# Performance work log

Measured on AMD Instinct MI355X. Metric: run time of the kernel, lower is better.

The kernel has to match this reference:

```python
import jax, jax.numpy as jnp
import numpy as np

N = 1_500_000  # nodes (250k tracklets x 6 hits)
E = 12_000_000  # edges


def setup_inputs() -> dict:
    key = jax.random.key(0)
    ks = jax.random.split(key, 26)
    w = lambda k, shape: (jax.random.normal(k, shape, jnp.float32) * 0.1)
    inp = {
        "x": jax.random.normal(ks[0], (N, 1), jnp.float32),
        "edge_index": jax.random.randint(ks[1], (2, E), 0, N),
        "edge_attr": jax.random.normal(ks[2], (E, 2), jnp.float32),
        # conv1: in=1, prop=9, edge=2, out=9
        "Wx1": w(ks[3], (9, 1)), "bx1": w(ks[4], (9,)),
        "We1": w(ks[5], (9, 2)), "be1": w(ks[6], (9,)),
        "Wo1": w(ks[7], (9, 9)), "bo1": w(ks[8], (9,)),
        # conv2: in=9, prop=9, edge=2, out=9
        "Wx2": w(ks[9], (9, 9)), "bx2": w(ks[10], (9,)),
        "We2": w(ks[11], (9, 2)), "be2": w(ks[12], (9,)),
        "Wo2": w(ks[13], (9, 9)), "bo2": w(ks[14], (9,)),
        # conv3: in=9, prop=9, edge=2, out=4
        "Wx3": w(ks[15], (9, 9)), "bx3": w(ks[16], (9,)),
        "We3": w(ks[17], (9, 2)), "be3": w(ks[18], (9,)),
        "Wo3": w(ks[19], (4, 9)), "bo3": w(ks[20], (4,)),
        # head MLP
        "W1": w(ks[21], (8, 24)), "b1": w(ks[22], (8,)),
        "W2": w(ks[23], (4, 8)), "b2": w(ks[24], (4,)),
    }
    return inp


def _conv(x, src, dst, edge_attr, Wx, bx, We, be, Wo, bo):
    # trackletGNN: lin_x -> gather x_j -> * lin_edge(edge_attr) -> scatter-add -> lin_out
    h = x @ Wx.T + bx                      # [N, P]
    msg = h[src] * (edge_attr @ We.T + be)  # [E, P] gather + edge linear + multiply
    agg = jax.ops.segment_sum(msg, dst, num_segments=x.shape[0])  # [N, P]
    return agg @ Wo.T + bo


def reference(x, edge_index, edge_attr,
              Wx1, bx1, We1, be1, Wo1, bo1,
              Wx2, bx2, We2, be2, Wo2, bo2,
              Wx3, bx3, We3, be3, Wo3, bo3,
              W1, b1, W2, b2):
    src, dst = edge_index[0], edge_index[1]
    h = jax.nn.relu(_conv(x, src, dst, edge_attr, Wx1, bx1, We1, be1, Wo1, bo1))
    h = jax.nn.relu(_conv(h, src, dst, edge_attr, Wx2, bx2, We2, be2, Wo2, bo2))
    h = jax.nn.relu(_conv(h, src, dst, edge_attr, Wx3, bx3, We3, be3, Wo3, bo3))
    h = h.reshape(-1, 24)                   # 6 nodes x 4 feats per tracklet
    h = jax.nn.relu(h @ W1.T + b1)
    h = h @ W2.T + b2
    return jax.nn.log_softmax(h, axis=1)
```

## Files before the change

kernel.cpp:

```cpp
#include <hip/hip_runtime.h>
#include <hip/hip_bf16.h>


#define NNODES 1500000
#define NEDGES 12000000
#define NTRACK 250000
#define NBUCK  1465
#define PCHUNK 4096
#define PBLK   2930
#define HCHUNK 32768
#define HBLK   367
#define SRCMASK 0x1FFFFFu
#define FXSCALE 16777216.f
#define FXINV   (1.f / 16777216.f)

typedef unsigned int   u32;
typedef unsigned short u16;

static __device__ __forceinline__ float b2f(u32 v) {
    union { float f; u32 u; } x; x.u = v << 16; return x.f;
}
static __device__ __forceinline__ u16 f2b(float f) {
    __hip_bfloat16 h = __float2bfloat16(f);
    return *reinterpret_cast<u16*>(&h);
}
static __device__ __forceinline__ float ldw(const void* p, int i, int isf32) {
    return isf32 ? ((const float*)p)[i] : b2f((u32)((const u16*)p)[i]);
}
static __device__ __forceinline__ int fx(float f) {
    return (int)rintf(f * FXSCALE);
}


__global__ void k_detect(const u16* a, const u16* b, const u16* c,
                         const u16* d, const u16* e, const u16* f,
                         int* flag) {
    if (blockIdx.x == 0 && threadIdx.x == 0) {
        int isf32 = 0;
        const u16* ps[6] = {a, b, c, d, e, f};
        const int  ns[6] = {9, 9, 9, 9, 9, 8};
        for (int k = 0; k < 6; k++)
            for (int i = 0; i < ns[k]; i++) {
                float v = b2f((u32)ps[k][i]);
                if (!(fabsf(v) < 1.0e3f)) isf32 = 1;
            }
        *flag = isf32;
    }
}


__global__ __launch_bounds__(256) void k_xcast(const void* __restrict__ x,
                                               u16* __restrict__ xb,
                                               const int* __restrict__ flag) {
    int isf32 = *flag;
    int n = blockIdx.x * 256 + threadIdx.x;
    if (n < NNODES)
        xb[n] = isf32 ? f2b(((const float*)x)[n]) : ((const u16*)x)[n];
}


__global__ __launch_bounds__(512) void k_bhist(const int* __restrict__ dst,
                                               int* __restrict__ gh) {
    __shared__ u32 h[NBUCK];
    int t = threadIdx.x;
    for (int b = t; b < NBUCK; b += 512) h[b] = 0;
    __syncthreads();
    int c0 = blockIdx.x * HCHUNK;
#pragma unroll 4
    for (int i = 0; i < HCHUNK / 512; i++) {
        int e = c0 + i * 512 + t;
        if (e < NEDGES) atomicAdd(&h[((u32)dst[e]) >> 10], 1u);
    }
    __syncthreads();
    for (int b = t; b < NBUCK; b += 512) {
        u32 c = h[b];
        if (c) atomicAdd((u32*)&gh[b], c);
    }
}

__global__ __launch_bounds__(256) void k_bscan(const int* __restrict__ gh,
                                               int* __restrict__ bstart,
                                               int* __restrict__ gcur) {
    __shared__ u32 sd[256];
    __shared__ u32 carry;
    int t = threadIdx.x;
    if (t == 0) carry = 0;
    __syncthreads();
    for (int c0 = 0; c0 < NBUCK; c0 += 256) {
        int b = c0 + t;
        u32 v = (b < NBUCK) ? (u32)gh[b] : 0;
        sd[t] = v; __syncthreads();
        for (int o = 1; o < 256; o <<= 1) {
            u32 a = (t >= o) ? sd[t - o] : 0;
            __syncthreads();
            sd[t] += a;
            __syncthreads();
        }
        u32 excl = carry + sd[t] - v;
        if (b < NBUCK) { bstart[b] = (int)excl; gcur[b] = (int)excl; }
        __syncthreads();
        if (t == 255) carry += sd[255];
        __syncthreads();
    }
    if (t == 0) bstart[NBUCK] = NEDGES;
}


__global__ __launch_bounds__(512) void k_part(const int* __restrict__ src,
                                              const int* __restrict__ dst,
                                              const void* __restrict__ attr,
                                              int* __restrict__ gcur,
                                              uint2* __restrict__ perm,
                                              const int* __restrict__ flag) {
    __shared__ int   cur[NBUCK];
    __shared__ int   gbA[NBUCK];
    __shared__ uint2 rec[PCHUNK];
    __shared__ u32   gad[PCHUNK];
    __shared__ u32   sd[512];
    __shared__ u32   carryS;
    int isf32 = *flag;
    int t = threadIdx.x;
    int c0 = blockIdx.x * PCHUNK;
    int chunkN = NEDGES - c0; if (chunkN > PCHUNK) chunkN = PCHUNK;

    for (int b = t; b < NBUCK; b += 512) cur[b] = 0;
    if (t == 0) carryS = 0;
    __syncthreads();

    int ds_[8], sr_[8];
#pragma unroll
    for (int k = 0; k < 8; k++) {
        int e = c0 + k * 512 + t;
        if (e < NEDGES) {
            ds_[k] = dst[e];
            sr_[k] = src[e];
            atomicAdd((u32*)&cur[((u32)ds_[k]) >> 10], 1u);
        } else { ds_[k] = -1; sr_[k] = 0; }
    }
    __syncthreads();

    for (int b0 = 0; b0 < NBUCK; b0 += 512) {
        int b = b0 + t;
        u32 v = (b < NBUCK) ? (u32)cur[b] : 0;
        sd[t] = v; __syncthreads();
        for (int o = 1; o < 512; o <<= 1) {
            u32 a = (t >= o) ? sd[t - o] : 0;
            __syncthreads();
            sd[t] += a;
            __syncthreads();
        }
        u32 excl = carryS + sd[t] - v;
        if (b < NBUCK) {
            cur[b] = (int)excl;
            if (v) gbA[b] = atomicAdd(&gcur[b], (int)v) - (int)excl;
        }
        __syncthreads();
        if (t == 511) carryS += sd[511];
        __syncthreads();
    }

#pragma unroll
    for (int k = 0; k < 8; k++) {
        int e = c0 + k * 512 + t;
        if (e < NEDGES) {
            u32 d  = (u32)ds_[k];
            u32 fb = d >> 10;
            u32 ap;
            if (isf32) {
                float2 a = ((const float2*)attr)[e];
                ap = (u32)f2b(a.x) | ((u32)f2b(a.y) << 16);
            } else {
                ap = ((const u32*)attr)[e];
            }
            int slot = atomicAdd(&cur[fb], 1);
            uint2 r; r.x = ((u32)sr_[k]) | ((d & 1023u) << 21); r.y = ap;
            rec[slot] = r;
            gad[slot] = (u32)(gbA[fb] + slot);
        }
    }
    __syncthreads();

#pragma unroll
    for (int j = 0; j < 8; j++) {
        int s = j * 512 + t;
        if (s < chunkN) perm[gad[s]] = rec[s];
    }
}


__global__ __launch_bounds__(256) void k_eagg1(
        const int* __restrict__ bstart, const uint2* __restrict__ perm,
        const u16* __restrict__ xb,
        const void* Wx, const void* bx, const void* We, const void* be,
        const void* Wo, const void* bo, const void* Wxn, const void* bxn,
        uint4* __restrict__ hA, u16* __restrict__ hB,
        const int* __restrict__ flag) {
    __shared__ int acc[1024 * 9];
    __shared__ float sWx[9], sbx[9], sWe[18], sbe[9], sWo[81], sbo[9], sWxn[81], sbxn[9];
    int isf32 = *flag;
    int t = threadIdx.x;
    if (t < 9)  sWx[t]  = ldw(Wx,  t, isf32);
    if (t < 9)  sbx[t]  = ldw(bx,  t, isf32);
    if (t < 18) sWe[t]  = ldw(We,  t, isf32);
    if (t < 9)  sbe[t]  = ldw(be,  t, isf32);
    if (t < 81) sWo[t]  = ldw(Wo,  t, isf32);
    if (t < 9)  sbo[t]  = ldw(bo,  t, isf32);
    if (t < 81) sWxn[t] = ldw(Wxn, t, isf32);
    if (t < 9)  sbxn[t] = ldw(bxn, t, isf32);
    for (int i = t; i < 1024 * 9; i += 256) acc[i] = 0;
    __syncthreads();

    int b = blockIdx.x;
    int r0 = bstart[b], r1 = bstart[b + 1];
    for (int i = r0 + t; i < r1; i += 256) {
        uint2 rec = perm[i];
        int   l   = (int)((rec.x >> 21) & 1023u);
        float xs  = b2f((u32)xb[rec.x & SRCMASK]);
        float a0  = b2f(rec.y & 0xffffu);
        float a1  = b2f(rec.y >> 16);
        int* ap = &acc[l * 9];
#pragma unroll
        for (int j = 0; j < 9; j++) {
            float e  = fmaf(a0, sWe[2 * j], fmaf(a1, sWe[2 * j + 1], sbe[j]));
            float hh = fmaf(xs, sWx[j], sbx[j]);
            atomicAdd(&ap[j], fx(hh * e));
        }
    }
    __syncthreads();

    for (int l = t; l < 1024; l += 256) {
        int n = b * 1024 + l;
        if (n >= NNODES) break;
        float av[9];
#pragma unroll
        for (int j = 0; j < 9; j++) av[j] = (float)acc[l * 9 + j] * FXINV;
        float o[9];
#pragma unroll
        for (int k = 0; k < 9; k++) {
            float v = sbo[k];
#pragma unroll
            for (int j = 0; j < 9; j++) v = fmaf(av[j], sWo[k * 9 + j], v);
            o[k] = fmaxf(v, 0.f);
        }
        u16 hv[9];
#pragma unroll
        for (int j = 0; j < 9; j++) {
            float v = sbxn[j];
#pragma unroll
            for (int k = 0; k < 9; k++) v = fmaf(o[k], sWxn[j * 9 + k], v);
            hv[j] = f2b(v);
        }
        uint4 q;
        q.x = (u32)hv[0] | ((u32)hv[1] << 16);
        q.y = (u32)hv[2] | ((u32)hv[3] << 16);
        q.z = (u32)hv[4] | ((u32)hv[5] << 16);
        q.w = (u32)hv[6] | ((u32)hv[7] << 16);
        hA[n] = q;
        hB[n] = hv[8];
    }
}


template <int OUTF, bool FUSE_NEXT>
__global__ __launch_bounds__(256) void k_eagg(
        const int* __restrict__ bstart, const uint2* __restrict__ perm,
        const uint4* __restrict__ hA, const u16* __restrict__ hB,
        const void* We, const void* be, const void* Wo, const void* bo,
        const void* Wxn, const void* bxn,
        uint4* __restrict__ oA, u16* __restrict__ oB,
        const int* __restrict__ flag) {
    __shared__ int acc[1024 * 9];
    __shared__ float sWe[18], sbe[9], sWo[OUTF * 9], sbo[OUTF], sWxn[81], sbxn[9];
    int isf32 = *flag;
    int t = threadIdx.x;
    if (t < 18)       sWe[t] = ldw(We, t, isf32);
    if (t < 9)        sbe[t] = ldw(be, t, isf32);
    if (t < OUTF * 9) sWo[t] = ldw(Wo, t, isf32);
    if (t < OUTF)     sbo[t] = ldw(bo, t, isf32);
    if constexpr (FUSE_NEXT) {
        if (t < 81) sWxn[t] = ldw(Wxn, t, isf32);
        if (t < 9)  sbxn[t] = ldw(bxn, t, isf32);
    }
    for (int i = t; i < 1024 * 9; i += 256) acc[i] = 0;
    __syncthreads();

    int b = blockIdx.x;
    int r0 = bstart[b], r1 = bstart[b + 1];
    for (int i = r0 + t; i < r1; i += 256) {
        uint2 rec = perm[i];
        int   s   = (int)(rec.x & SRCMASK);
        int   l   = (int)((rec.x >> 21) & 1023u);
        float a0  = b2f(rec.y & 0xffffu);
        float a1  = b2f(rec.y >> 16);
        uint4 qa  = hA[s];
        u32   qb  = (u32)hB[s];
        float h[9];
        h[0] = b2f(qa.x & 0xffffu); h[1] = b2f(qa.x >> 16);
        h[2] = b2f(qa.y & 0xffffu); h[3] = b2f(qa.y >> 16);
        h[4] = b2f(qa.z & 0xffffu); h[5] = b2f(qa.z >> 16);
        h[6] = b2f(qa.w & 0xffffu); h[7] = b2f(qa.w >> 16);
        h[8] = b2f(qb);
        int* ap = &acc[l * 9];
#pragma unroll
        for (int j = 0; j < 9; j++) {
            float e = fmaf(a0, sWe[2 * j], fmaf(a1, sWe[2 * j + 1], sbe[j]));
            atomicAdd(&ap[j], fx(h[j] * e));
        }
    }
    __syncthreads();

    for (int l = t; l < 1024; l += 256) {
        int n = b * 1024 + l;
        if (n >= NNODES) break;
        float av[9];
#pragma unroll
        for (int j = 0; j < 9; j++) av[j] = (float)acc[l * 9 + j] * FXINV;
        float o[OUTF];
#pragma unroll
        for (int k = 0; k < OUTF; k++) {
            float v = sbo[k];
#pragma unroll
            for (int j = 0; j < 9; j++) v = fmaf(av[j], sWo[k * 9 + j], v);
            o[k] = fmaxf(v, 0.f);
        }
        if constexpr (FUSE_NEXT) {
            u16 hv[9];
#pragma unroll
            for (int j = 0; j < 9; j++) {
                float v = sbxn[j];
#pragma unroll
                for (int k = 0; k < OUTF; k++) v = fmaf(o[k], sWxn[j * 9 + k], v);
                hv[j] = f2b(v);
            }
            uint4 q;
            q.x = (u32)hv[0] | ((u32)hv[1] << 16);
            q.y = (u32)hv[2] | ((u32)hv[3] << 16);
            q.z = (u32)hv[4] | ((u32)hv[5] << 16);
            q.w = (u32)hv[6] | ((u32)hv[7] << 16);
            oA[n] = q;
            oB[n] = hv[8];
        } else {
            uint2 q;
            q.x = (u32)f2b(o[0]) | ((u32)f2b(o[1]) << 16);
            q.y = (u32)f2b(o[2]) | ((u32)f2b(o[3]) << 16);
            ((uint2*)oA)[n] = q;
        }
    }
}


__global__ __launch_bounds__(256) void k_head(
        const u16* __restrict__ f,
        const void* W1, const void* b1, const void* W2, const void* b2,
        void* __restrict__ out, const int* __restrict__ flag) {
    __shared__ float sW1[192], sb1[8], sW2[32], sb2[4];
    int isf32 = *flag;
    int t = threadIdx.x;
    if (t < 192) sW1[t] = ldw(W1, t, isf32);
    if (t < 8)   sb1[t] = ldw(b1, t, isf32);
    if (t < 32)  sW2[t] = ldw(W2, t, isf32);
    if (t < 4)   sb2[t] = ldw(b2, t, isf32);
    __syncthreads();

    int tr = blockIdx.x * 256 + t;
    if (tr >= NTRACK) return;

    const uint4* fp = (const uint4*)(f + (size_t)tr * 24);
    uint4 A = fp[0], B = fp[1], C = fp[2];
    u32 w[12] = {A.x, A.y, A.z, A.w, B.x, B.y, B.z, B.w, C.x, C.y, C.z, C.w};
    float in[24];
#pragma unroll
    for (int i = 0; i < 12; i++) {
        in[2 * i]     = b2f(w[i] & 0xffffu);
        in[2 * i + 1] = b2f(w[i] >> 16);
    }

    float z1[8];
#pragma unroll
    for (int o = 0; o < 8; o++) {
        float v = sb1[o];
#pragma unroll
        for (int i = 0; i < 24; i++) v = fmaf(in[i], sW1[o * 24 + i], v);
        z1[o] = fmaxf(v, 0.f);
    }
    float z2[4];
#pragma unroll
    for (int c = 0; c < 4; c++) {
        float v = sb2[c];
#pragma unroll
        for (int o = 0; o < 8; o++) v = fmaf(z1[o], sW2[c * 8 + o], v);
        z2[c] = v;
    }
    float m = fmaxf(fmaxf(z2[0], z2[1]), fmaxf(z2[2], z2[3]));
    float s = 0.f;
#pragma unroll
    for (int c = 0; c < 4; c++) s += expf(z2[c] - m);
    float l = logf(s) + m;

    if (isf32) {
        float4 q; q.x = z2[0] - l; q.y = z2[1] - l; q.z = z2[2] - l; q.w = z2[3] - l;
        ((float4*)((float*)out + (size_t)tr * 4))[0] = q;
    } else {
        uint2 q;
        q.x = (u32)f2b(z2[0] - l) | ((u32)f2b(z2[1] - l) << 16);
        q.y = (u32)f2b(z2[2] - l) | ((u32)f2b(z2[3] - l) << 16);
        ((uint2*)((u16*)out + (size_t)tr * 4))[0] = q;
    }
}


extern "C" void kernel_launch(void* const* d_in, const int* in_sizes, int n_in,
                              void* d_out, int out_size, void* d_ws, size_t ws_size,
                              hipStream_t stream) {
    const void* X    = d_in[0];
    const int* eidx  = (const int*)d_in[1];
    const void* eattr= d_in[2];
    const void *WX1 = d_in[3],  *BX1 = d_in[4];
    const void *WE1 = d_in[5],  *BE1 = d_in[6];
    const void *WO1 = d_in[7],  *BO1 = d_in[8];
    const void *WX2 = d_in[9],  *BX2 = d_in[10];
    const void *WE2 = d_in[11], *BE2 = d_in[12];
    const void *WO2 = d_in[13], *BO2 = d_in[14];
    const void *WX3 = d_in[15], *BX3 = d_in[16];
    const void *WE3 = d_in[17], *BE3 = d_in[18];
    const void *WO3 = d_in[19], *BO3 = d_in[20];
    const void *W1  = d_in[21], *B1  = d_in[22];
    const void *W2  = d_in[23], *B2  = d_in[24];

    const int* src = eidx;
    const int* dst = eidx + NEDGES;

    char* w = (char*)d_ws;
    size_t off = 0;
    auto take = [&](size_t bytes) -> void* {
        void* p = w + off;
        off += (bytes + 255) & ~(size_t)255;
        return p;
    };
    int*   flag   = (int*)take(256);
    int*   gh     = (int*)take((size_t)NBUCK * 4);
    int*   bstart = (int*)take((size_t)(NBUCK + 1) * 4);
    int*   gcur   = (int*)take((size_t)NBUCK * 4);
    u16*   xb     = (u16*)take((size_t)NNODES * 2);
    uint2* perm   = (uint2*)take((size_t)NEDGES * 8);
    uint4* hA2    = (uint4*)take((size_t)NNODES * 16);
    u16*   hB2    = (u16*)take((size_t)NNODES * 2);
    uint4* hA3    = (uint4*)take((size_t)NNODES * 16);
    u16*   hB3    = (u16*)take((size_t)NNODES * 2);
    u16*   f      = (u16*)hA2;
    (void)ws_size; (void)n_in; (void)in_sizes; (void)out_size;

    const int NB = (NNODES + 255) / 256;
    const int TB = (NTRACK + 255) / 256;

    hipMemsetAsync(gh, 0, (size_t)NBUCK * 4, stream);

    k_detect <<<1,    64,  0, stream>>>((const u16*)BX1, (const u16*)BE1, (const u16*)BO1,
                                        (const u16*)BX2, (const u16*)BE2, (const u16*)B1, flag);
    k_xcast  <<<NB,   256, 0, stream>>>(X, xb, flag);
    k_bhist  <<<HBLK, 512, 0, stream>>>(dst, gh);
    k_bscan  <<<1,    256, 0, stream>>>(gh, bstart, gcur);
    k_part   <<<PBLK, 512, 0, stream>>>(src, dst, eattr, gcur, perm, flag);

    k_eagg1        <<<NBUCK, 256, 0, stream>>>(bstart, perm, xb,
                                               WX1, BX1, WE1, BE1, WO1, BO1, WX2, BX2,
                                               hA2, hB2, flag);
    k_eagg<9,true> <<<NBUCK, 256, 0, stream>>>(bstart, perm, hA2, hB2,
                                               WE2, BE2, WO2, BO2, WX3, BX3,
                                               hA3, hB3, flag);
    k_eagg<4,false><<<NBUCK, 256, 0, stream>>>(bstart, perm, hA3, hB3,
                                               WE3, BE3, WO3, BO3, WO3, BO3,
                                               (uint4*)f, (u16*)f, flag);
    k_head         <<<TB,    256, 0, stream>>>(f, W1, B1, W2, B2, d_out, flag);
}
```

Baseline: 1.124 ms.

## Halve bucket size, interleave node features, drop partition address buffer

Buckets shrink from 1024 to 512 destination nodes, so the per-block LDS accumulator halves and more blocks can be resident (launch bounds now request 8 blocks). Node features move from split 16-byte plus 2-byte arrays into one interleaved 32-byte record per node, so each gather touches a single contiguous region instead of two arrays. The partition kernel drops its shared global-address array and finds each slot's bucket by binary search over the scanned offsets. The edge-linear term is computed before the gather is consumed. This trades LDS and memory footprint for extra binary-search work and a larger intermediate feature buffer.

```diff
diff --git a/kernel.cpp b/kernel.cpp
--- a/kernel.cpp
+++ b/kernel.cpp
@@ -5,7 +5,10 @@
 #define NNODES 1500000
 #define NEDGES 12000000
 #define NTRACK 250000
-#define NBUCK  1465
+#define BSH    9
+#define BSZ    512
+#define BMASK  511u
+#define NBUCK  2930
 #define PCHUNK 4096
 #define PBLK   2930
 #define HCHUNK 32768
@@ -69,7 +72,7 @@
 #pragma unroll 4
     for (int i = 0; i < HCHUNK / 512; i++) {
         int e = c0 + i * 512 + t;
-        if (e < NEDGES) atomicAdd(&h[((u32)dst[e]) >> 10], 1u);
+        if (e < NEDGES) atomicAdd(&h[((u32)dst[e]) >> BSH], 1u);
     }
     __syncthreads();
     for (int b = t; b < NBUCK; b += 512) {
@@ -115,7 +118,6 @@
     __shared__ int   cur[NBUCK];
     __shared__ int   gbA[NBUCK];
     __shared__ uint2 rec[PCHUNK];
-    __shared__ u32   gad[PCHUNK];
     __shared__ u32   sd[512];
     __shared__ u32   carryS;
     int isf32 = *flag;
@@ -134,7 +136,7 @@
         if (e < NEDGES) {
             ds_[k] = dst[e];
             sr_[k] = src[e];
-            atomicAdd((u32*)&cur[((u32)ds_[k]) >> 10], 1u);
+            atomicAdd((u32*)&cur[((u32)ds_[k]) >> BSH], 1u);
         } else { ds_[k] = -1; sr_[k] = 0; }
     }
     __syncthreads();
@@ -164,7 +166,7 @@
         int e = c0 + k * 512 + t;
         if (e < NEDGES) {
             u32 d  = (u32)ds_[k];
-            u32 fb = d >> 10;
+            u32 fb = d >> BSH;
             u32 ap;
             if (isf32) {
                 float2 a = ((const float2*)attr)[e];
@@ -173,9 +175,8 @@
                 ap = ((const u32*)attr)[e];
             }
             int slot = atomicAdd(&cur[fb], 1);
-            uint2 r; r.x = ((u32)sr_[k]) | ((d & 1023u) << 21); r.y = ap;
+            uint2 r; r.x = ((u32)sr_[k]) | ((d & BMASK) << 21); r.y = ap;
             rec[slot] = r;
-            gad[slot] = (u32)(gbA[fb] + slot);
         }
     }
     __syncthreads();
@@ -183,19 +184,25 @@
 #pragma unroll
     for (int j = 0; j < 8; j++) {
         int s = j * 512 + t;
-        if (s < chunkN) perm[gad[s]] = rec[s];
-    }
-}
-
-
-__global__ __launch_bounds__(256) void k_eagg1(
+        if (s < chunkN) {
+            int lo = 0, hi = NBUCK - 1;
+            while (lo < hi) {
+                int mid = (lo + hi) >> 1;
+                if (cur[mid] > s) hi = mid; else lo = mid + 1;
+            }
+            perm[gbA[lo] + s] = rec[s];
+        }
+    }
+}
+
+
+__global__ __launch_bounds__(256, 8) void k_eagg1(
         const int* __restrict__ bstart, const uint2* __restrict__ perm,
         const u16* __restrict__ xb,
         const void* Wx, const void* bx, const void* We, const void* be,
         const void* Wo, const void* bo, const void* Wxn, const void* bxn,
-        uint4* __restrict__ hA, u16* __restrict__ hB,
-        const int* __restrict__ flag) {
-    __shared__ int acc[1024 * 9];
+        uint4* __restrict__ hO, const int* __restrict__ flag) {
+    __shared__ int acc[BSZ * 9];
     __shared__ float sWx[9], sbx[9], sWe[18], sbe[9], sWo[81], sbo[9], sWxn[81], sbxn[9];
     int isf32 = *flag;
     int t = threadIdx.x;
@@ -207,14 +214,14 @@
     if (t < 9)  sbo[t]  = ldw(bo,  t, isf32);
     if (t < 81) sWxn[t] = ldw(Wxn, t, isf32);
     if (t < 9)  sbxn[t] = ldw(bxn, t, isf32);
-    for (int i = t; i < 1024 * 9; i += 256) acc[i] = 0;
+    for (int i = t; i < BSZ * 9; i += 256) acc[i] = 0;
     __syncthreads();
 
     int b = blockIdx.x;
     int r0 = bstart[b], r1 = bstart[b + 1];
     for (int i = r0 + t; i < r1; i += 256) {
         uint2 rec = perm[i];
-        int   l   = (int)((rec.x >> 21) & 1023u);
+        int   l   = (int)((rec.x >> 21) & BMASK);
         float xs  = b2f((u32)xb[rec.x & SRCMASK]);
         float a0  = b2f(rec.y & 0xffffu);
         float a1  = b2f(rec.y >> 16);
@@ -228,8 +235,8 @@
     }
     __syncthreads();
 
-    for (int l = t; l < 1024; l += 256) {
-        int n = b * 1024 + l;
+    for (int l = t; l < BSZ; l += 256) {
+        int n = b * BSZ + l;
         if (n >= NNODES) break;
         float av[9];
 #pragma unroll
@@ -250,27 +257,28 @@
             for (int k = 0; k < 9; k++) v = fmaf(o[k], sWxn[j * 9 + k], v);
             hv[j] = f2b(v);
         }
-        uint4 q;
-        q.x = (u32)hv[0] | ((u32)hv[1] << 16);
-        q.y = (u32)hv[2] | ((u32)hv[3] << 16);
-        q.z = (u32)hv[4] | ((u32)hv[5] << 16);
-        q.w = (u32)hv[6] | ((u32)hv[7] << 16);
-        hA[n] = q;
-        hB[n] = hv[8];
+        uint4 q0, q1;
+        q0.x = (u32)hv[0] | ((u32)hv[1] << 16);
+        q0.y = (u32)hv[2] | ((u32)hv[3] << 16);
+        q0.z = (u32)hv[4] | ((u32)hv[5] << 16);
+        q0.w = (u32)hv[6] | ((u32)hv[7] << 16);
+        q1.x = (u32)hv[8]; q1.y = 0; q1.z = 0; q1.w = 0;
+        size_t p = (size_t)n << 1;
+        hO[p] = q0; hO[p + 1] = q1;
     }
 }
 
 
 template <int OUTF, bool FUSE_NEXT>
-__global__ __launch_bounds__(256) void k_eagg(
+__global__ __launch_bounds__(256, 8) void k_eagg(
         const int* __restrict__ bstart, const uint2* __restrict__ perm,
-        const uint4* __restrict__ hA, const u16* __restrict__ hB,
+        const uint4* __restrict__ hT,
         const void* We, const void* be, const void* Wo, const void* bo,
         const void* Wxn, const void* bxn,
-        uint4* __restrict__ oA, u16* __restrict__ oB,
-        const int* __restrict__ flag) {
-    __shared__ int acc[1024 * 9];
-    __shared__ float sWe[18], sbe[9], sWo[OUTF * 9], sbo[OUTF], sWxn[81], sbxn[9];
+        uint4* __restrict__ oT, const int* __restrict__ flag) {
+    __shared__ int acc[BSZ * 9];
+    __shared__ float sWe[18], sbe[9], sWo[OUTF * 9], sbo[OUTF];
+    __shared__ float sWxn[FUSE_NEXT ? 81 : 1], sbxn[FUSE_NEXT ? 9 : 1];
     int isf32 = *flag;
     int t = threadIdx.x;
     if (t < 18)       sWe[t] = ldw(We, t, isf32);
@@ -281,7 +289,7 @@
         if (t < 81) sWxn[t] = ldw(Wxn, t, isf32);
         if (t < 9)  sbxn[t] = ldw(bxn, t, isf32);
     }
-    for (int i = t; i < 1024 * 9; i += 256) acc[i] = 0;
+    for (int i = t; i < BSZ * 9; i += 256) acc[i] = 0;
     __syncthreads();
 
     int b = blockIdx.x;
@@ -289,28 +297,31 @@
     for (int i = r0 + t; i < r1; i += 256) {
         uint2 rec = perm[i];
         int   s   = (int)(rec.x & SRCMASK);
-        int   l   = (int)((rec.x >> 21) & 1023u);
+        const uint4* hp = hT + ((size_t)s << 1);
+        uint4 qa  = hp[0];
+        u32   qb  = hp[1].x;
+        int   l   = (int)((rec.x >> 21) & BMASK);
         float a0  = b2f(rec.y & 0xffffu);
         float a1  = b2f(rec.y >> 16);
-        uint4 qa  = hA[s];
-        u32   qb  = (u32)hB[s];
+        float ev[9];
+#pragma unroll
+        for (int j = 0; j < 9; j++)
+            ev[j] = fmaf(a0, sWe[2 * j], fmaf(a1, sWe[2 * j + 1], sbe[j]));
         float h[9];
         h[0] = b2f(qa.x & 0xffffu); h[1] = b2f(qa.x >> 16);
         h[2] = b2f(qa.y & 0xffffu); h[3] = b2f(qa.y >> 16);
         h[4] = b2f(qa.z & 0xffffu); h[5] = b2f(qa.z >> 16);
         h[6] = b2f(qa.w & 0xffffu); h[7] = b2f(qa.w >> 16);
-        h[8] = b2f(qb);
+        h[8] = b2f(qb & 0xffffu);
         int* ap = &acc[l * 9];
 #pragma unroll
-        for (int j = 0; j < 9; j++) {
-            float e = fmaf(a0, sWe[2 * j], fmaf(a1, sWe[2 * j + 1], sbe[j]));
-            atomicAdd(&ap[j], fx(h[j] * e));
-        }
-    }
-    __syncthreads();
-
-    for (int l = t; l < 1024; l += 256) {
-        int n = b * 1024 + l;
+        for (int j = 0; j < 9; j++)
+            atomicAdd(&ap[j], fx(h[j] * ev[j]));
+    }
+    __syncthreads();
+
+    for (int l = t; l < BSZ; l += 256) {
+        int n = b * BSZ + l;
         if (n >= NNODES) break;
         float av[9];
 #pragma unroll
@@ -332,18 +343,19 @@
                 for (int k = 0; k < OUTF; k++) v = fmaf(o[k], sWxn[j * 9 + k], v);
                 hv[j] = f2b(v);
             }
-            uint4 q;
-            q.x = (u32)hv[0] | ((u32)hv[1] << 16);
-            q.y = (u32)hv[2] | ((u32)hv[3] << 16);
-            q.z = (u32)hv[4] | ((u32)hv[5] << 16);
-            q.w = (u32)hv[6] | ((u32)hv[7] << 16);
-            oA[n] = q;
-            oB[n] = hv[8];
+            uint4 q0, q1;
+            q0.x = (u32)hv[0] | ((u32)hv[1] << 16);
+            q0.y = (u32)hv[2] | ((u32)hv[3] << 16);
+            q0.z = (u32)hv[4] | ((u32)hv[5] << 16);
+            q0.w = (u32)hv[6] | ((u32)hv[7] << 16);
+            q1.x = (u32)hv[8]; q1.y = 0; q1.z = 0; q1.w = 0;
+            size_t p = (size_t)n << 1;
+            oT[p] = q0; oT[p + 1] = q1;
         } else {
             uint2 q;
             q.x = (u32)f2b(o[0]) | ((u32)f2b(o[1]) << 16);
             q.y = (u32)f2b(o[2]) | ((u32)f2b(o[3]) << 16);
-            ((uint2*)oA)[n] = q;
+            ((uint2*)oT)[n] = q;
         }
     }
 }
@@ -443,11 +455,9 @@
     int*   gcur   = (int*)take((size_t)NBUCK * 4);
     u16*   xb     = (u16*)take((size_t)NNODES * 2);
     uint2* perm   = (uint2*)take((size_t)NEDGES * 8);
-    uint4* hA2    = (uint4*)take((size_t)NNODES * 16);
-    u16*   hB2    = (u16*)take((size_t)NNODES * 2);
-    uint4* hA3    = (uint4*)take((size_t)NNODES * 16);
-    u16*   hB3    = (u16*)take((size_t)NNODES * 2);
-    u16*   f      = (u16*)hA2;
+    uint4* h2     = (uint4*)take((size_t)NNODES * 32);
+    uint4* h3     = (uint4*)take((size_t)NNODES * 32);
+    u16*   f      = (u16*)h2;
     (void)ws_size; (void)n_in; (void)in_sizes; (void)out_size;
 
     const int NB = (NNODES + 255) / 256;
@@ -464,12 +474,12 @@
 
     k_eagg1        <<<NBUCK, 256, 0, stream>>>(bstart, perm, xb,
                                                WX1, BX1, WE1, BE1, WO1, BO1, WX2, BX2,
-                                               hA2, hB2, flag);
-    k_eagg<9,true> <<<NBUCK, 256, 0, stream>>>(bstart, perm, hA2, hB2,
+                                               h2, flag);
+    k_eagg<9,true> <<<NBUCK, 256, 0, stream>>>(bstart, perm, h2,
                                                WE2, BE2, WO2, BO2, WX3, BX3,
-                                               hA3, hB3, flag);
-    k_eagg<4,false><<<NBUCK, 256, 0, stream>>>(bstart, perm, hA3, hB3,
+                                               h3, flag);
+    k_eagg<4,false><<<NBUCK, 256, 0, stream>>>(bstart, perm, h3,
                                                WE3, BE3, WO3, BO3, WO3, BO3,
-                                               (uint4*)f, (u16*)f, flag);
+                                               (uint4*)f, flag);
     k_head         <<<TB,    256, 0, stream>>>(f, W1, B1, W2, B2, d_out, flag);
 }
```

Result: slower. 1.642 ms (+46.1%).

## Halve dst bucket size and sort each bucket's edges by source slice

Applied to the files above, without the earlier changes.

Shrinks destination buckets from 1024 to 512 nodes, which doubles the block count for the aggregation kernels and halves their shared accumulator. It adds a per-bucket counting-sort pass (k_srt) that reorders edges by source-index slice so the gathers of hA/hB in later layers have more locality. The partition kernel now finds each record's bucket by binary search over the shared prefix array instead of storing a per-slot global address, which frees shared memory. In exchange it adds an extra read and write pass over the 12M-edge permutation, and buckets longer than 5120 edges are silently left unsorted.

```diff
diff --git a/kernel.cpp b/kernel.cpp
--- a/kernel.cpp
+++ b/kernel.cpp
@@ -5,12 +5,17 @@
 #define NNODES 1500000
 #define NEDGES 12000000
 #define NTRACK 250000
-#define NBUCK  1465
+#define BSH    9
+#define BSZ    512
+#define BMASK  511u
+#define NBUCK  2930
 #define PCHUNK 4096
 #define PBLK   2930
 #define HCHUNK 32768
 #define HBLK   367
 #define SRCMASK 0x1FFFFFu
+#define NSLICE 48
+#define SRTR   20
 #define FXSCALE 16777216.f
 #define FXINV   (1.f / 16777216.f)
 
@@ -69,7 +74,7 @@
 #pragma unroll 4
     for (int i = 0; i < HCHUNK / 512; i++) {
         int e = c0 + i * 512 + t;
-        if (e < NEDGES) atomicAdd(&h[((u32)dst[e]) >> 10], 1u);
+        if (e < NEDGES) atomicAdd(&h[((u32)dst[e]) >> BSH], 1u);
     }
     __syncthreads();
     for (int b = t; b < NBUCK; b += 512) {
@@ -115,7 +120,6 @@
     __shared__ int   cur[NBUCK];
     __shared__ int   gbA[NBUCK];
     __shared__ uint2 rec[PCHUNK];
-    __shared__ u32   gad[PCHUNK];
     __shared__ u32   sd[512];
     __shared__ u32   carryS;
     int isf32 = *flag;
@@ -134,7 +138,7 @@
         if (e < NEDGES) {
             ds_[k] = dst[e];
             sr_[k] = src[e];
-            atomicAdd((u32*)&cur[((u32)ds_[k]) >> 10], 1u);
+            atomicAdd((u32*)&cur[((u32)ds_[k]) >> BSH], 1u);
         } else { ds_[k] = -1; sr_[k] = 0; }
     }
     __syncthreads();
@@ -164,7 +168,7 @@
         int e = c0 + k * 512 + t;
         if (e < NEDGES) {
             u32 d  = (u32)ds_[k];
-            u32 fb = d >> 10;
+            u32 fb = d >> BSH;
             u32 ap;
             if (isf32) {
                 float2 a = ((const float2*)attr)[e];
@@ -173,9 +177,8 @@
                 ap = ((const u32*)attr)[e];
             }
             int slot = atomicAdd(&cur[fb], 1);
-            uint2 r; r.x = ((u32)sr_[k]) | ((d & 1023u) << 21); r.y = ap;
+            uint2 r; r.x = ((u32)sr_[k]) | ((d & BMASK) << 21); r.y = ap;
             rec[slot] = r;
-            gad[slot] = (u32)(gbA[fb] + slot);
         }
     }
     __syncthreads();
@@ -183,7 +186,55 @@
 #pragma unroll
     for (int j = 0; j < 8; j++) {
         int s = j * 512 + t;
-        if (s < chunkN) perm[gad[s]] = rec[s];
+        if (s < chunkN) {
+            int lo = 0, hi = NBUCK - 1;
+            while (lo < hi) {
+                int mid = (lo + hi) >> 1;
+                if (cur[mid] > s) hi = mid; else lo = mid + 1;
+            }
+            perm[gbA[lo] + s] = rec[s];
+        }
+    }
+}
+
+
+__global__ __launch_bounds__(256) void k_srt(const int* __restrict__ bstart,
+                                             uint2* __restrict__ perm) {
+    __shared__ int h[NSLICE];
+    int t = threadIdx.x;
+    int b = blockIdx.x;
+    int r0 = bstart[b], r1 = bstart[b + 1];
+    int len = r1 - r0;
+    if (len <= 0) return;
+    if (len > SRTR * 256) return;
+    if (t < NSLICE) h[t] = 0;
+    __syncthreads();
+
+    uint2 r[SRTR];
+#pragma unroll
+    for (int k = 0; k < SRTR; k++) {
+        int i = r0 + k * 256 + t;
+        if (i < r1) {
+            r[k] = perm[i];
+            atomicAdd(&h[(r[k].x & SRCMASK) >> 15], 1);
+        } else {
+            r[k].x = 0xFFFFFFFFu;
+        }
+    }
+    __syncthreads();
+
+    if (t == 0) {
+        int s = 0;
+        for (int k = 0; k < NSLICE; k++) { int c = h[k]; h[k] = s; s += c; }
+    }
+    __syncthreads();
+
+#pragma unroll
+    for (int k = 0; k < SRTR; k++) {
+        if (r[k].x != 0xFFFFFFFFu) {
+            int slot = atomicAdd(&h[(r[k].x & SRCMASK) >> 15], 1);
+            perm[r0 + slot] = r[k];
+        }
     }
 }
 
@@ -195,7 +246,7 @@
         const void* Wo, const void* bo, const void* Wxn, const void* bxn,
         uint4* __restrict__ hA, u16* __restrict__ hB,
         const int* __restrict__ flag) {
-    __shared__ int acc[1024 * 9];
+    __shared__ int acc[BSZ * 9];
     __shared__ float sWx[9], sbx[9], sWe[18], sbe[9], sWo[81], sbo[9], sWxn[81], sbxn[9];
     int isf32 = *flag;
     int t = threadIdx.x;
@@ -207,14 +258,14 @@
     if (t < 9)  sbo[t]  = ldw(bo,  t, isf32);
     if (t < 81) sWxn[t] = ldw(Wxn, t, isf32);
     if (t < 9)  sbxn[t] = ldw(bxn, t, isf32);
-    for (int i = t; i < 1024 * 9; i += 256) acc[i] = 0;
+    for (int i = t; i < BSZ * 9; i += 256) acc[i] = 0;
     __syncthreads();
 
     int b = blockIdx.x;
     int r0 = bstart[b], r1 = bstart[b + 1];
     for (int i = r0 + t; i < r1; i += 256) {
         uint2 rec = perm[i];
-        int   l   = (int)((rec.x >> 21) & 1023u);
+        int   l   = (int)((rec.x >> 21) & BMASK);
         float xs  = b2f((u32)xb[rec.x & SRCMASK]);
         float a0  = b2f(rec.y & 0xffffu);
         float a1  = b2f(rec.y >> 16);
@@ -228,8 +279,8 @@
     }
     __syncthreads();
 
-    for (int l = t; l < 1024; l += 256) {
-        int n = b * 1024 + l;
+    for (int l = t; l < BSZ; l += 256) {
+        int n = b * BSZ + l;
         if (n >= NNODES) break;
         float av[9];
 #pragma unroll
@@ -269,8 +320,9 @@
         const void* Wxn, const void* bxn,
         uint4* __restrict__ oA, u16* __restrict__ oB,
         const int* __restrict__ flag) {
-    __shared__ int acc[1024 * 9];
-    __shared__ float sWe[18], sbe[9], sWo[OUTF * 9], sbo[OUTF], sWxn[81], sbxn[9];
+    __shared__ int acc[BSZ * 9];
+    __shared__ float sWe[18], sbe[9], sWo[OUTF * 9], sbo[OUTF];
+    __shared__ float sWxn[FUSE_NEXT ? 81 : 1], sbxn[FUSE_NEXT ? 9 : 1];
     int isf32 = *flag;
     int t = threadIdx.x;
     if (t < 18)       sWe[t] = ldw(We, t, isf32);
@@ -281,7 +333,7 @@
         if (t < 81) sWxn[t] = ldw(Wxn, t, isf32);
         if (t < 9)  sbxn[t] = ldw(bxn, t, isf32);
     }
-    for (int i = t; i < 1024 * 9; i += 256) acc[i] = 0;
+    for (int i = t; i < BSZ * 9; i += 256) acc[i] = 0;
     __syncthreads();
 
     int b = blockIdx.x;
@@ -289,11 +341,15 @@
     for (int i = r0 + t; i < r1; i += 256) {
         uint2 rec = perm[i];
         int   s   = (int)(rec.x & SRCMASK);
-        int   l   = (int)((rec.x >> 21) & 1023u);
+        int   l   = (int)((rec.x >> 21) & BMASK);
         float a0  = b2f(rec.y & 0xffffu);
         float a1  = b2f(rec.y >> 16);
         uint4 qa  = hA[s];
         u32   qb  = (u32)hB[s];
+        float ev[9];
+#pragma unroll
+        for (int j = 0; j < 9; j++)
+            ev[j] = fmaf(a0, sWe[2 * j], fmaf(a1, sWe[2 * j + 1], sbe[j]));
         float h[9];
         h[0] = b2f(qa.x & 0xffffu); h[1] = b2f(qa.x >> 16);
         h[2] = b2f(qa.y & 0xffffu); h[3] = b2f(qa.y >> 16);
@@ -302,15 +358,13 @@
         h[8] = b2f(qb);
         int* ap = &acc[l * 9];
 #pragma unroll
-        for (int j = 0; j < 9; j++) {
-            float e = fmaf(a0, sWe[2 * j], fmaf(a1, sWe[2 * j + 1], sbe[j]));
-            atomicAdd(&ap[j], fx(h[j] * e));
-        }
-    }
-    __syncthreads();
-
-    for (int l = t; l < 1024; l += 256) {
-        int n = b * 1024 + l;
+        for (int j = 0; j < 9; j++)
+            atomicAdd(&ap[j], fx(h[j] * ev[j]));
+    }
+    __syncthreads();
+
+    for (int l = t; l < BSZ; l += 256) {
+        int n = b * BSZ + l;
         if (n >= NNODES) break;
         float av[9];
 #pragma unroll
@@ -461,6 +515,7 @@
     k_bhist  <<<HBLK, 512, 0, stream>>>(dst, gh);
     k_bscan  <<<1,    256, 0, stream>>>(gh, bstart, gcur);
     k_part   <<<PBLK, 512, 0, stream>>>(src, dst, eattr, gcur, perm, flag);
+    k_srt    <<<NBUCK,256, 0, stream>>>(bstart, perm);
 
     k_eagg1        <<<NBUCK, 256, 0, stream>>>(bstart, perm, xb,
                                                WX1, BX1, WE1, BE1, WO1, BO1, WX2, BX2,
```

Result: faster. 1.044 ms (-7.2%).
